# Kernel optimization log

Measured on AMD Instinct MI355X. Metric: run time of the kernel, lower is better.

## Reference

```python
import jax, jax.numpy as jnp
import numpy as np

E = 256      # embedding_dim
H = 16       # head_num
D = 16       # qkv_dim
FF = 512     # ff_hidden_dim
L = 5        # encoder_layer_num
B = 4        # batch
N = 256      # node_cnt
EPS = 1e-5   # InstanceNorm eps


def setup_inputs() -> dict:
    key = jax.random.key(0)
    ks = jax.random.split(key, 16)
    s = 0.05

    def nrm(k, shape):
        return jax.random.normal(k, shape, dtype=jnp.float32) * s

    return {
        "data": jax.random.normal(ks[0], (B, N, N), dtype=jnp.float32),
        "node_rand": jax.random.uniform(ks[1], (B, N, 1), dtype=jnp.float32),
        # Cross_Encoder input projections (Linear(1, E))
        "Wnode": nrm(ks[2], (1, E)), "bnode": jnp.zeros((E,), jnp.float32),
        "Wedge": nrm(ks[3], (1, E)), "bedge": jnp.zeros((E,), jnp.float32),
        # Per layer (L) x per block (2: row/col) weights
        "Wq": nrm(ks[4], (L, 2, E, H * D)),
        "Wk": nrm(ks[5], (L, 2, E, H * D)),
        "Wv": nrm(ks[6], (L, 2, E, H * D)),
        "Wcomb": nrm(ks[7], (L, 2, H * D, E)),
        "bcomb": jnp.zeros((L, 2, E), jnp.float32),
        "n1w": jnp.ones((L, 2, E), jnp.float32),
        "n1b": jnp.zeros((L, 2, E), jnp.float32),
        "W1": nrm(ks[8], (L, 2, E, FF)),
        "b1": jnp.zeros((L, 2, FF), jnp.float32),
        "W2": nrm(ks[9], (L, 2, FF, E)),
        "b2": jnp.zeros((L, 2, E), jnp.float32),
        "n2w": jnp.ones((L, 2, E), jnp.float32),
        "n2b": jnp.zeros((L, 2, E), jnp.float32),
        # MixedScore edge-bias projection per block: E -> H channels
        "Wmix": nrm(ks[10], (L, 2, E, H)),
    }


def _instance_norm(x, w, b):
    # x: [B, N, E]; InstanceNorm1d after transpose -> normalize over node dim N per (B, channel)
    mu = jnp.mean(x, axis=1, keepdims=True)
    var = jnp.var(x, axis=1, keepdims=True)
    return (x - mu) * jax.lax.rsqrt(var + EPS) * w + b


def reference(data, node_rand, Wnode, bnode, Wedge, bedge,
              Wq, Wk, Wv, Wcomb, bcomb, n1w, n1b,
              W1, b1, W2, b2, n2w, n2b, Wmix):
    inv_sqrt_d = jnp.float32(1.0) / jnp.sqrt(jnp.float32(D))

    def block(row, col, edge, i, j):
        # row, col: [B, N, E]; edge: [B, N, N, E]
        q = (row @ Wq[i, j]).reshape(B, N, H, D)
        k = (col @ Wk[i, j]).reshape(B, N, H, D)
        v = (col @ Wv[i, j]).reshape(B, N, H, D)
        score = jnp.einsum('bnhd,bmhd->bhnm', q, k) * inv_sqrt_d
        score = score + jnp.einsum('bnme,eh->bhnm', edge, Wmix[i, j])
        w = jax.nn.softmax(score, axis=-1)
        out = jnp.einsum('bhnm,bmhd->bnhd', w, v).reshape(B, N, H * D)
        mh = out @ Wcomb[i, j] + bcomb[i, j]
        o1 = _instance_norm(row + mh, n1w[i, j], n1b[i, j])
        ff = jax.nn.relu(o1 @ W1[i, j] + b1[i, j]) @ W2[i, j] + b2[i, j]
        return _instance_norm(o1 + ff, n2w[i, j], n2b[i, j])

    # compute_normalized_matrices: per-batch global min-max scaling
    flat = data.reshape(B, -1)
    mn = flat.min(axis=1).reshape(B, 1, 1)
    mx = flat.max(axis=1).reshape(B, 1, 1)
    rng = mx - mn
    rng = jnp.where(rng == 0, jnp.float32(1.0), rng)
    scaled = (data - mn) / rng

    edge = scaled[..., None] @ Wedge + bedge           # [B, N, N, E]
    emb = node_rand @ Wnode + bnode                    # [B, N, E]

    row, col = emb, emb
    for i in range(L):
        row_new = block(row, col, edge, i, 0)
        col = block(col, row, jnp.swapaxes(edge, 1, 2), i, 1)
        row = row_new
    return row, col
```

## Files before the change

### kernel.cpp

```cpp
#include <hip/hip_runtime.h>
#include <hip/hip_bf16.h>

#define E 256
#define H 16
#define DD 16
#define FFH 512
#define LAYERS 5
#define BB 4
#define NN 256
#define MROWS 1024

typedef __attribute__((ext_vector_type(8))) short bfrag;
typedef __attribute__((ext_vector_type(4))) float f32x4;
typedef __attribute__((ext_vector_type(8))) unsigned short us8;
typedef unsigned short u16;

__device__ __forceinline__ void bsplit(float v, u16& h, u16& l) {
    unsigned u = __float_as_uint(v);
    u16 hh = (u16)((u + 0x7fffu + ((u >> 16) & 1u)) >> 16);
    float r = v - __uint_as_float((unsigned)hh << 16);
    unsigned u2 = __float_as_uint(r);
    h = hh;
    l = (u16)((u2 + 0x7fffu + ((u2 >> 16) & 1u)) >> 16);
}

union PrepS {
    float tile[32 * 33];
    struct { u16 th[64 * 40], tl[64 * 40]; } wp;
    struct { float smin[4], smax[4]; } mm;
};

__global__ __launch_bounds__(256) void k_prep(
    const float* __restrict__ data, const float* __restrict__ node_rand,
    const float* __restrict__ Wnode, const float* __restrict__ bnode,
    const float* __restrict__ Wedge, const float* __restrict__ bedge,
    const float* __restrict__ Wmix,
    const float* __restrict__ Wq, const float* __restrict__ Wk, const float* __restrict__ Wv,
    const float* __restrict__ Wc, const float* __restrict__ W1, const float* __restrict__ W2,
    float* __restrict__ pmin, float* __restrict__ pmax, float* __restrict__ c1c0,
    float* __restrict__ rowb, float* __restrict__ colb,
    u16* rowh, u16* rowl, u16* colh, u16* coll,
    float* __restrict__ dataT,
    u16* qh, u16* ql, u16* kh, u16* kl_, u16* vh, u16* vl,
    u16* ch, u16* cl, u16* f1h, u16* f1l, u16* f2h, u16* f2l) {
    __shared__ PrepS ps;
    int bid = blockIdx.x;
    int t = threadIdx.x;
    if (bid < 64) {
        int b = bid >> 4, p = bid & 15;
        const float* src = data + (size_t)b * NN * NN + p * 4096;
        float lmin = 1e30f, lmax = -1e30f;
        #pragma unroll
        for (int i = 0; i < 16; i++) {
            float v = src[t + i * 256];
            lmin = fminf(lmin, v);
            lmax = fmaxf(lmax, v);
        }
        #pragma unroll
        for (int off = 32; off; off >>= 1) {
            lmin = fminf(lmin, __shfl_down(lmin, off));
            lmax = fmaxf(lmax, __shfl_down(lmax, off));
        }
        int wid = t >> 6, lane = t & 63;
        if (lane == 0) { ps.mm.smin[wid] = lmin; ps.mm.smax[wid] = lmax; }
        __syncthreads();
        if (t == 0) {
            pmin[b * 16 + p] = fminf(fminf(ps.mm.smin[0], ps.mm.smin[1]), fminf(ps.mm.smin[2], ps.mm.smin[3]));
            pmax[b * 16 + p] = fmaxf(fmaxf(ps.mm.smax[0], ps.mm.smax[1]), fmaxf(ps.mm.smax[2], ps.mm.smax[3]));
        }
    } else if (bid < 1088) {
        int idx = (bid - 64) * 256 + t;
        int bn = idx >> 8, e = idx & 255;
        float v = node_rand[bn] * Wnode[e] + bnode[e];
        rowb[idx] = v;
        colb[idx] = v;
        u16 h, l;
        bsplit(v, h, l);
        rowh[idx] = h; rowl[idx] = l;
        colh[idx] = h; coll[idx] = l;
    } else if (bid < 1344) {
        int local = bid - 1088;
        int bx = local & 7, by = (local >> 3) & 7, b = local >> 6;
        int r0 = by * 32, c0 = bx * 32;
        int tx = t & 31, ty = t >> 5;
        const float* src = data + (size_t)b * NN * NN;
        float* dst = dataT + (size_t)b * NN * NN;
        #pragma unroll
        for (int i = 0; i < 4; i++)
            ps.tile[(ty + 8 * i) * 33 + tx] = src[(size_t)(r0 + ty + 8 * i) * NN + c0 + tx];
        __syncthreads();
        #pragma unroll
        for (int i = 0; i < 4; i++)
            dst[(size_t)(c0 + ty + 8 * i) * NN + r0 + tx] = ps.tile[tx * 33 + ty + 8 * i];
    } else if (bid < 3904) {
        int id = bid - 1344;
        const float* W; u16 *Dh, *Dl; int K, N, mat, s, nt;
        if (id < 1280) {
            int seg = id / 320, local = id % 320;
            mat = local >> 5; int rem = local & 31; s = rem >> 2; nt = rem & 3;
            K = 256; N = 256;
            W  = seg == 0 ? Wq : seg == 1 ? Wk : seg == 2 ? Wv : Wc;
            Dh = seg == 0 ? qh : seg == 1 ? kh : seg == 2 ? vh : ch;
            Dl = seg == 0 ? ql : seg == 1 ? kl_ : seg == 2 ? vl : cl;
        } else if (id < 1920) {
            int local = id - 1280;
            mat = local >> 6; int rem = local & 63; s = rem >> 3; nt = rem & 7;
            K = 256; N = 512; W = W1; Dh = f1h; Dl = f1l;
        } else {
            int local = id - 1920;
            mat = local >> 6; int rem = local & 63; s = rem >> 2; nt = rem & 3;
            K = 512; N = 256; W = W2; Dh = f2h; Dl = f2l;
        }
        int kk = t >> 3, nl = (t & 7) * 8;
        const float* p = W + (size_t)mat * K * N + (size_t)(s * 32 + kk) * N + nt * 64 + nl;
        float4 f0 = *(const float4*)p;
        float4 f1v = *(const float4*)(p + 4);
        float fv[8] = {f0.x, f0.y, f0.z, f0.w, f1v.x, f1v.y, f1v.z, f1v.w};
        #pragma unroll
        for (int i = 0; i < 8; i++) bsplit(fv[i], ps.wp.th[(nl + i) * 40 + kk], ps.wp.tl[(nl + i) * 40 + kk]);
        __syncthreads();
        int n = t >> 2, ko = (t & 3) * 8;
        size_t dbase = (size_t)mat * K * N + (size_t)s * N * 32 + (size_t)nt * 64 * 32
                     + (size_t)n * 32 + ko;
        *(us8*)(Dh + dbase) = *(const us8*)&ps.wp.th[n * 40 + ko];
        *(us8*)(Dl + dbase) = *(const us8*)&ps.wp.tl[n * 40 + ko];
    } else {
        if (t < LAYERS * 2 * H) {
            int lj = t >> 4, h = t & 15;
            float c1 = 0.f, c0 = 0.f;
            for (int e = 0; e < E; e++) {
                float wm = Wmix[(lj * E + e) * H + h];
                c1 += Wedge[e] * wm;
                c0 += bedge[e] * wm;
            }
            c1c0[t] = c1;
            c1c0[160 + t] = c0;
        }
    }
}

__device__ __forceinline__ void mfma_gemm(const u16* __restrict__ Ah, const u16* __restrict__ Al,
                                          const u16* __restrict__ Bh, const u16* __restrict__ Bl,
                                          const float* __restrict__ bias, const float* __restrict__ R,
                                          float* __restrict__ Cf, u16* __restrict__ Ch,
                                          u16* __restrict__ Cl, int K, int Ncols, int relu) {
    __shared__ u16 AsH[32 * 136], AsL[32 * 136], BsH[64 * 136], BsL[64 * 136];
    int t = threadIdx.x;
    int lane = t & 63, wave = t >> 6;
    int quad = lane >> 4, l16 = lane & 15;
    int wy = wave >> 1, wx = wave & 1;
    int mBase = blockIdx.x * 32, nBase = blockIdx.y * 64;
    f32x4 acc0 = {0.f, 0.f, 0.f, 0.f}, acc1 = acc0;
    int arow = t >> 3, ak = (t & 7) * 16;
    int bcol = lane, bq = wave;
    const int nslab = K >> 7;
    const u16* apH = Ah + (size_t)(mBase + arow) * K + ak;
    const u16* apL = Al + (size_t)(mBase + arow) * K + ak;
    const size_t sstr = (size_t)Ncols * 32;
    size_t bbase = (size_t)bq * sstr + (size_t)(nBase + bcol) * 32;
    const u16* bpH = Bh + bbase;
    const u16* bpL = Bl + bbase;
    us8 rah0 = *(const us8*)apH, rah1 = *(const us8*)(apH + 8);
    us8 ral0 = *(const us8*)apL, ral1 = *(const us8*)(apL + 8);
    us8 rbh0 = *(const us8*)(bpH + 0);
    us8 rbh1 = *(const us8*)(bpH + 8);
    us8 rbh2 = *(const us8*)(bpH + 16);
    us8 rbh3 = *(const us8*)(bpH + 24);
    us8 rbl0 = *(const us8*)(bpL + 0);
    us8 rbl1 = *(const us8*)(bpL + 8);
    us8 rbl2 = *(const us8*)(bpL + 16);
    us8 rbl3 = *(const us8*)(bpL + 24);
    for (int s = 0; s < nslab; s++) {
        __syncthreads();
        *(us8*)&AsH[arow * 136 + ak] = rah0;  *(us8*)&AsH[arow * 136 + ak + 8] = rah1;
        *(us8*)&AsL[arow * 136 + ak] = ral0;  *(us8*)&AsL[arow * 136 + ak + 8] = ral1;
        {
            int bb = bcol * 136 + bq * 32;
            *(us8*)&BsH[bb + 0] = rbh0;  *(us8*)&BsH[bb + 8] = rbh1;
            *(us8*)&BsH[bb + 16] = rbh2; *(us8*)&BsH[bb + 24] = rbh3;
            *(us8*)&BsL[bb + 0] = rbl0;  *(us8*)&BsL[bb + 8] = rbl1;
            *(us8*)&BsL[bb + 16] = rbl2; *(us8*)&BsL[bb + 24] = rbl3;
        }
        __syncthreads();
        if (s + 1 < nslab) {
            rah0 = *(const us8*)(apH + (s + 1) * 128);
            rah1 = *(const us8*)(apH + (s + 1) * 128 + 8);
            ral0 = *(const us8*)(apL + (s + 1) * 128);
            ral1 = *(const us8*)(apL + (s + 1) * 128 + 8);
            const u16* nbH = bpH + (size_t)(4 * (s + 1)) * sstr;
            const u16* nbL = bpL + (size_t)(4 * (s + 1)) * sstr;
            rbh0 = *(const us8*)(nbH + 0);  rbh1 = *(const us8*)(nbH + 8);
            rbh2 = *(const us8*)(nbH + 16); rbh3 = *(const us8*)(nbH + 24);
            rbl0 = *(const us8*)(nbL + 0);  rbl1 = *(const us8*)(nbL + 8);
            rbl2 = *(const us8*)(nbL + 16); rbl3 = *(const us8*)(nbL + 24);
        }
        #pragma unroll
        for (int c = 0; c < 4; c++) {
            bfrag a_h = *(const bfrag*)&AsH[(wy * 16 + l16) * 136 + c * 32 + quad * 8];
            bfrag a_l = *(const bfrag*)&AsL[(wy * 16 + l16) * 136 + c * 32 + quad * 8];
            bfrag b_h0 = *(const bfrag*)&BsH[(wx * 32 + l16) * 136 + c * 32 + quad * 8];
            bfrag b_h1 = *(const bfrag*)&BsH[(wx * 32 + 16 + l16) * 136 + c * 32 + quad * 8];
            bfrag b_l0 = *(const bfrag*)&BsL[(wx * 32 + l16) * 136 + c * 32 + quad * 8];
            bfrag b_l1 = *(const bfrag*)&BsL[(wx * 32 + 16 + l16) * 136 + c * 32 + quad * 8];
            acc0 = __builtin_amdgcn_mfma_f32_16x16x32_bf16(a_h, b_h0, acc0, 0, 0, 0);
            acc1 = __builtin_amdgcn_mfma_f32_16x16x32_bf16(a_h, b_h1, acc1, 0, 0, 0);
            acc0 = __builtin_amdgcn_mfma_f32_16x16x32_bf16(a_h, b_l0, acc0, 0, 0, 0);
            acc1 = __builtin_amdgcn_mfma_f32_16x16x32_bf16(a_h, b_l1, acc1, 0, 0, 0);
            acc0 = __builtin_amdgcn_mfma_f32_16x16x32_bf16(a_l, b_h0, acc0, 0, 0, 0);
            acc1 = __builtin_amdgcn_mfma_f32_16x16x32_bf16(a_l, b_h1, acc1, 0, 0, 0);
        }
    }
    int col0 = nBase + wx * 32 + l16;
    int col1 = col0 + 16;
    float bia0 = bias ? bias[col0] : 0.f;
    float bia1 = bias ? bias[col1] : 0.f;
    #pragma unroll
    for (int r = 0; r < 4; r++) {
        int row0 = mBase + wy * 16 + quad * 4 + r;
        float v0 = acc0[r] + bia0, v1 = acc1[r] + bia1;
        if (R) {
            v0 += R[(size_t)row0 * Ncols + col0];
            v1 += R[(size_t)row0 * Ncols + col1];
        }
        if (relu) {
            v0 = fmaxf(v0, 0.f); v1 = fmaxf(v1, 0.f);
        }
        if (Cf) {
            Cf[(size_t)row0 * Ncols + col0] = v0;
            Cf[(size_t)row0 * Ncols + col1] = v1;
        } else {
            u16 h, l;
            bsplit(v0, h, l); Ch[(size_t)row0 * Ncols + col0] = h; Cl[(size_t)row0 * Ncols + col0] = l;
            bsplit(v1, h, l); Ch[(size_t)row0 * Ncols + col1] = h; Cl[(size_t)row0 * Ncols + col1] = l;
        }
    }
}

__global__ __launch_bounds__(256) void k_qkv(const u16* __restrict__ rowh, const u16* __restrict__ rowl,
                                             const u16* __restrict__ colh, const u16* __restrict__ coll,
                                             const u16* __restrict__ WqTh, const u16* __restrict__ WqTl,
                                             const u16* __restrict__ WkTh, const u16* __restrict__ WkTl,
                                             const u16* __restrict__ WvTh, const u16* __restrict__ WvTl,
                                             int lb2,
                                             u16* qhh0, u16* qhl0, u16* khh0, u16* khl0, u16* vhh0, u16* vhl0,
                                             u16* qhh1, u16* qhl1, u16* khh1, u16* khl1, u16* vhh1, u16* vhl1) {
    int z = blockIdx.z;
    int j = z / 3, w = z % 3;
    const u16* Ah = (w == 0) ? (j ? colh : rowh) : (j ? rowh : colh);
    const u16* Al = (w == 0) ? (j ? coll : rowl) : (j ? rowl : coll);
    const u16* Wh = (w == 0 ? WqTh : (w == 1 ? WkTh : WvTh)) + (size_t)(lb2 + j) * E * E;
    const u16* Wl = (w == 0 ? WqTl : (w == 1 ? WkTl : WvTl)) + (size_t)(lb2 + j) * E * E;
    u16* outs_h[6] = {qhh0, khh0, vhh0, qhh1, khh1, vhh1};
    u16* outs_l[6] = {qhl0, khl0, vhl0, qhl1, khl1, vhl1};
    mfma_gemm(Ah, Al, Wh, Wl, nullptr, nullptr, nullptr, outs_h[z], outs_l[z], E, E, 0);
}

__global__ __launch_bounds__(256) void k_mgemm(const u16* Ah0, const u16* Al0,
                                               const u16* Ah1, const u16* Al1,
                                               const u16* __restrict__ Bh, const u16* __restrict__ Bl,
                                               int lb2, long wstride,
                                               const float* __restrict__ biasl, int bstride,
                                               const float* R0, const float* R1,
                                               float* Cf0, float* Cf1,
                                               u16* Ch0, u16* Cl0, u16* Ch1, u16* Cl1,
                                               int K, int Ncols, int relu) {
    int j = blockIdx.z;
    mfma_gemm(j ? Ah1 : Ah0, j ? Al1 : Al0,
              Bh + (size_t)(lb2 + j) * wstride, Bl + (size_t)(lb2 + j) * wstride,
              biasl ? biasl + (size_t)j * bstride : nullptr,
              R0 ? (j ? R1 : R0) : nullptr,
              Cf0 ? (j ? Cf1 : Cf0) : nullptr,
              Ch0 ? (j ? Ch1 : Ch0) : nullptr,
              Cl0 ? (j ? Cl1 : Cl0) : nullptr,
              K, Ncols, relu);
}

__global__ __launch_bounds__(256) void k_attn(
    const u16* __restrict__ qh0, const u16* __restrict__ ql0,
    const u16* __restrict__ kh0, const u16* __restrict__ kl0,
    const u16* __restrict__ vh0, const u16* __restrict__ vl0,
    const u16* __restrict__ qh1, const u16* __restrict__ ql1,
    const u16* __restrict__ kh1, const u16* __restrict__ kl1,
    const u16* __restrict__ vh1, const u16* __restrict__ vl1,
    const float* __restrict__ data, const float* __restrict__ dataT,
    const float* __restrict__ pmin, const float* __restrict__ pmax,
    const float* __restrict__ c1c0, int lj_base,
    u16* __restrict__ atth0, u16* __restrict__ attl0,
    u16* __restrict__ atth1, u16* __restrict__ attl1) {
    __shared__ u16 Ks[256 * 40];
    __shared__ u16 VTh[16 * 264];
    __shared__ u16 VTl[16 * 264];
    __shared__ u16 Pw[4][2 * 16 * 40];

    int wgid = blockIdx.x;
    int r8 = wgid & 7;
    int qd = wgid >> 3;
    int nq = qd & 3;
    int bhj = r8 * 16 + (qd >> 2);
    int bh = bhj >> 1;
    int j = bhj & 1;
    int b = bh >> 4, h = bh & 15;
    const u16* qh = j ? qh1 : qh0;
    const u16* ql = j ? ql1 : ql0;
    const u16* kh = j ? kh1 : kh0;
    const u16* kl = j ? kl1 : kl0;
    const u16* vh = j ? vh1 : vh0;
    const u16* vl = j ? vl1 : vl0;
    float mn = 1e30f, mx = -1e30f;
    #pragma unroll
    for (int p = 0; p < 16; p++) {
        mn = fminf(mn, pmin[b * 16 + p]);
        mx = fmaxf(mx, pmax[b * 16 + p]);
    }
    float rng = mx - mn;
    if (rng == 0.f) rng = 1.f;
    float inv = 1.f / rng;
    float c1p = inv * c1c0[(lj_base + j) * 16 + h];
    float c0p = c1c0[160 + (lj_base + j) * 16 + h] - mn * c1p;

    int t = threadIdx.x;
    int lane = t & 63, w = t >> 6;
    int l16 = lane & 15, g = lane >> 4;
    int nb = nq * 64 + w * 16;
    int n = nb + l16;

    bfrag qbh, qbl;
    {
        size_t qoff = ((size_t)(b * NN + n) * E) + h * DD + (g & 1) * 8;
        qbh = *(const bfrag*)(qh + qoff);
        if (g < 2) {
            qbl = *(const bfrag*)(ql + qoff);
        } else {
            qbl = (bfrag)(short)0;
        }
    }

    {
        size_t roff = ((size_t)(b * NN + t) * E) + h * DD;
        us8 a = *(const us8*)(kh + roff);
        us8 bv = *(const us8*)(kh + roff + 8);
        us8 c = *(const us8*)(kl + roff);
        us8 d = *(const us8*)(kl + roff + 8);
        *(us8*)&Ks[t * 40 + 0] = a;   *(us8*)&Ks[t * 40 + 8] = bv;
        *(us8*)&Ks[t * 40 + 16] = c;  *(us8*)&Ks[t * 40 + 24] = d;
        us8 vh0v = *(const us8*)(vh + roff);
        us8 vh1v = *(const us8*)(vh + roff + 8);
        us8 vl0v = *(const us8*)(vl + roff);
        us8 vl1v = *(const us8*)(vl + roff + 8);
        #pragma unroll
        for (int d2 = 0; d2 < 8; d2++) {
            VTh[d2 * 264 + t] = vh0v[d2];
            VTh[(d2 + 8) * 264 + t] = vh1v[d2];
            VTl[d2 * 264 + t] = vl0v[d2];
            VTl[(d2 + 8) * 264 + t] = vl1v[d2];
        }
    }
    __syncthreads();

    const float* pedge = (j ? dataT : data) + (size_t)b * NN * NN + (size_t)n * NN;
    u16* myPh = &Pw[w][0];
    u16* myPl = &Pw[w][16 * 40];
    f32x4 oacc = {0.f, 0.f, 0.f, 0.f};
    float sum = 0.f;
    int aoff = g * 8;

    for (int c = 0; c < 8; c++) {
        #pragma unroll
        for (int tt = 0; tt < 2; tt++) {
            int mt = c * 2 + tt;
            int mrow = mt * 16 + l16;
            bfrag a1 = *(const bfrag*)&Ks[mrow * 40 + aoff];
            f32x4 sacc = {0.f, 0.f, 0.f, 0.f};
            sacc = __builtin_amdgcn_mfma_f32_16x16x32_bf16(a1, qbh, sacc, 0, 0, 0);
            sacc = __builtin_amdgcn_mfma_f32_16x16x32_bf16(a1, qbl, sacc, 0, 0, 0);
            float4 ev = *(const float4*)&pedge[mt * 16 + g * 4];
            float evf[4] = {ev.x, ev.y, ev.z, ev.w};
            u16 ph[4], pl[4];
            #pragma unroll
            for (int r = 0; r < 4; r++) {
                float s = sacc[r] * 0.25f + evf[r] * c1p + c0p;
                float e = __expf(s);
                sum += e;
                bsplit(e, ph[r], pl[r]);
            }
            ushort4 phv; phv.x = ph[0]; phv.y = ph[1]; phv.z = ph[2]; phv.w = ph[3];
            ushort4 plv; plv.x = pl[0]; plv.y = pl[1]; plv.z = pl[2]; plv.w = pl[3];
            *(ushort4*)&myPh[l16 * 40 + tt * 16 + g * 4] = phv;
            *(ushort4*)&myPl[l16 * 40 + tt * 16 + g * 4] = plv;
        }
        bfrag pbh = *(const bfrag*)&myPh[l16 * 40 + g * 8];
        bfrag pbl = *(const bfrag*)&myPl[l16 * 40 + g * 8];
        bfrag vah = *(const bfrag*)&VTh[l16 * 264 + c * 32 + g * 8];
        bfrag vaL = *(const bfrag*)&VTl[l16 * 264 + c * 32 + g * 8];
        oacc = __builtin_amdgcn_mfma_f32_16x16x32_bf16(vah, pbh, oacc, 0, 0, 0);
        oacc = __builtin_amdgcn_mfma_f32_16x16x32_bf16(vah, pbl, oacc, 0, 0, 0);
        oacc = __builtin_amdgcn_mfma_f32_16x16x32_bf16(vaL, pbh, oacc, 0, 0, 0);
    }
    sum += __shfl_xor(sum, 16);
    sum += __shfl_xor(sum, 32);
    float invs = 1.f / sum;
    u16 hh[4], ll[4];
    #pragma unroll
    for (int r = 0; r < 4; r++) bsplit(oacc[r] * invs, hh[r], ll[r]);
    size_t obase = ((size_t)(b * NN + n) * E) + h * DD + g * 4;
    u16* oh = (j ? atth1 : atth0) + obase;
    u16* ol = (j ? attl1 : attl0) + obase;
    ushort4 ohv; ohv.x = hh[0]; ohv.y = hh[1]; ohv.z = hh[2]; ohv.w = hh[3];
    ushort4 olv; olv.x = ll[0]; olv.y = ll[1]; olv.z = ll[2]; olv.w = ll[3];
    *(ushort4*)oh = ohv;
    *(ushort4*)ol = olv;
}

__global__ __launch_bounds__(256) void k_inorm(const float* __restrict__ Y0, const float* __restrict__ Y1,
                                               const float* __restrict__ wl, const float* __restrict__ bl,
                                               int pstride,
                                               float* Of0, float* Of1,
                                               u16* Oh0, u16* Ol0, u16* Oh1, u16* Ol1,
                                               float* __restrict__ fout) {
    int b = blockIdx.x, j = blockIdx.y;
    int ec = blockIdx.z * 8;
    const float* Y = (j ? Y1 : Y0) + (size_t)b * NN * E;
    float* O = (j ? Of1 : Of0) + (size_t)b * NN * E;
    u16* Oh = (j ? Oh1 : Oh0) + (size_t)b * NN * E;
    u16* Ol = (j ? Ol1 : Ol0) + (size_t)b * NN * E;
    const float* w = wl + (size_t)j * pstride;
    const float* bb = bl + (size_t)j * pstride;
    int t = threadIdx.x;
    int et = t & 7, n0 = t >> 3;
    int e = ec + et;
    float vals[8];
    float s = 0.f, s2 = 0.f;
    #pragma unroll
    for (int kk = 0; kk < 8; kk++) {
        float v = Y[(size_t)(n0 + 32 * kk) * E + e];
        vals[kk] = v;
        s += v;
        s2 += v * v;
    }
    __shared__ float ps[32 * 9], ps2[32 * 9];
    ps[n0 * 9 + et] = s;
    ps2[n0 * 9 + et] = s2;
    __syncthreads();
    float st = 0.f, st2 = 0.f;
    #pragma unroll
    for (int kk = 0; kk < 32; kk++) { st += ps[kk * 9 + et]; st2 += ps2[kk * 9 + et]; }
    float mu = st * (1.f / NN);
    float var = fmaxf(st2 * (1.f / NN) - mu * mu, 0.f);
    float scale = w[e] * rsqrtf(var + 1e-5f);
    float shift = bb[e] - mu * scale;
    #pragma unroll
    for (int kk = 0; kk < 8; kk++) {
        float vv = vals[kk] * scale + shift;
        size_t idx = (size_t)(n0 + 32 * kk) * E + e;
        O[idx] = vv;
        u16 hh, ll;
        bsplit(vv, hh, ll);
        Oh[idx] = hh;
        Ol[idx] = ll;
        if (fout) fout[(size_t)j * (BB * NN * E) + (size_t)b * NN * E + idx] = vv;
    }
}


extern "C" void kernel_launch(void* const* d_in, const int* in_sizes, int n_in,
                              void* d_out, int out_size, void* d_ws, size_t ws_size,
                              hipStream_t stream) {
    const float* data      = (const float*)d_in[0];
    const float* node_rand = (const float*)d_in[1];
    const float* Wnode     = (const float*)d_in[2];
    const float* bnode     = (const float*)d_in[3];
    const float* Wedge     = (const float*)d_in[4];
    const float* bedge     = (const float*)d_in[5];
    const float* Wq        = (const float*)d_in[6];
    const float* Wk        = (const float*)d_in[7];
    const float* Wv        = (const float*)d_in[8];
    const float* Wcomb     = (const float*)d_in[9];
    const float* bcomb     = (const float*)d_in[10];
    const float* n1w       = (const float*)d_in[11];
    const float* n1b       = (const float*)d_in[12];
    const float* W1        = (const float*)d_in[13];
    const float* b1        = (const float*)d_in[14];
    const float* W2        = (const float*)d_in[15];
    const float* b2        = (const float*)d_in[16];
    const float* n2w       = (const float*)d_in[17];
    const float* n2b       = (const float*)d_in[18];
    const float* Wmix      = (const float*)d_in[19];
    float* out = (float*)d_out;

    float* ws = (float*)d_ws;
    const size_t T = (size_t)MROWS * E;
    const size_t TF = (size_t)MROWS * FFH;
    float* dataT = ws + 0 * T;
    float* row   = ws + 1 * T;
    float* col   = ws + 2 * T;
    float* q0    = ws + 3 * T;
    float* q1    = ws + 4 * T;
    float* o1f0  = ws + 9 * T;
    float* o1f1  = ws + 10 * T;
    float* pmin  = ws + 11 * T;
    float* pmax  = pmin + 64;
    float* c1c0  = pmax + 64;
    u16* us = (u16*)(ws + 11 * T + 512);
    auto nxt = [&](size_t n) { u16* p = us; us += n; return p; };
    u16* rowh = nxt(T);  u16* rowl = nxt(T);
    u16* colh = nxt(T);  u16* coll = nxt(T);
    u16* atth0 = nxt(T); u16* attl0 = nxt(T);
    u16* atth1 = nxt(T); u16* attl1 = nxt(T);
    u16* o1h0 = nxt(T);  u16* o1l0 = nxt(T);
    u16* o1h1 = nxt(T);  u16* o1l1 = nxt(T);
    u16* ffhh0 = nxt(TF); u16* ffhl0 = nxt(TF);
    u16* ffhh1 = nxt(TF); u16* ffhl1 = nxt(TF);
    const size_t EE10 = (size_t)10 * E * E;
    const size_t EF10 = (size_t)10 * E * FFH;
    u16* WqTh = nxt(EE10); u16* WqTl = nxt(EE10);
    u16* WkTh = nxt(EE10); u16* WkTl = nxt(EE10);
    u16* WvTh = nxt(EE10); u16* WvTl = nxt(EE10);
    u16* WcTh = nxt(EE10); u16* WcTl = nxt(EE10);
    u16* W1Th = nxt(EF10); u16* W1Tl = nxt(EF10);
    u16* W2Th = nxt(EF10); u16* W2Tl = nxt(EF10);
    u16* qhh0 = nxt(T); u16* qhl0 = nxt(T);
    u16* khh0 = nxt(T); u16* khl0 = nxt(T);
    u16* vhh0 = nxt(T); u16* vhl0 = nxt(T);
    u16* qhh1 = nxt(T); u16* qhl1 = nxt(T);
    u16* khh1 = nxt(T); u16* khl1 = nxt(T);
    u16* vhh1 = nxt(T); u16* vhl1 = nxt(T);
    float* y0 = q0;   float* y1 = q1;
    float* y20 = q0;  float* y21 = q1;

    k_prep<<<3905, 256, 0, stream>>>(data, node_rand, Wnode, bnode,
                                     Wedge, bedge, Wmix,
                                     Wq, Wk, Wv, Wcomb, W1, W2,
                                     pmin, pmax, c1c0,
                                     row, col, rowh, rowl, colh, coll, dataT,
                                     WqTh, WqTl, WkTh, WkTl, WvTh, WvTl,
                                     WcTh, WcTl, W1Th, W1Tl, W2Th, W2Tl);

    for (int l = 0; l < LAYERS; l++) {
        int lb2 = l * 2;
        k_qkv<<<dim3(32, 4, 6), 256, 0, stream>>>(rowh, rowl, colh, coll,
                                                  WqTh, WqTl, WkTh, WkTl, WvTh, WvTl, lb2,
                                                  qhh0, qhl0, khh0, khl0, vhh0, vhl0,
                                                  qhh1, qhl1, khh1, khl1, vhh1, vhl1);
        k_attn<<<dim3(512), 256, 0, stream>>>(qhh0, qhl0, khh0, khl0, vhh0, vhl0,
                                              qhh1, qhl1, khh1, khl1, vhh1, vhl1,
                                              data, dataT, pmin, pmax, c1c0, lb2,
                                              atth0, attl0, atth1, attl1);
        k_mgemm<<<dim3(32, 4, 2), 256, 0, stream>>>(atth0, attl0, atth1, attl1,
                                                    WcTh, WcTl, lb2, (long)E * E,
                                                    bcomb, E,
                                                    row, col, y0, y1,
                                                    nullptr, nullptr, nullptr, nullptr,
                                                    E, E, 0);
        k_inorm<<<dim3(BB, 2, 32), 256, 0, stream>>>(y0, y1,
                                                     n1w + (size_t)lb2 * E, n1b + (size_t)lb2 * E, E,
                                                     o1f0, o1f1, o1h0, o1l0, o1h1, o1l1, nullptr);
        k_mgemm<<<dim3(32, 8, 2), 256, 0, stream>>>(o1h0, o1l0, o1h1, o1l1,
                                                    W1Th, W1Tl, lb2, (long)E * FFH,
                                                    b1, FFH,
                                                    nullptr, nullptr, nullptr, nullptr,
                                                    ffhh0, ffhl0, ffhh1, ffhl1,
                                                    E, FFH, 1);
        k_mgemm<<<dim3(32, 4, 2), 256, 0, stream>>>(ffhh0, ffhl0, ffhh1, ffhl1,
                                                    W2Th, W2Tl, lb2, (long)FFH * E,
                                                    b2, E,
                                                    o1f0, o1f1, q0 , q1 ,
                                                    nullptr, nullptr, nullptr, nullptr,
                                                    FFH, E, 0);
        k_inorm<<<dim3(BB, 2, 32), 256, 0, stream>>>(y20, y21,
                                                     n2w + (size_t)lb2 * E, n2b + (size_t)lb2 * E, E,
                                                     row, col, rowh, rowl, colh, coll,
                                                     (l == LAYERS - 1) ? out : nullptr);
    }
}
```

Before: 370.6 us.

## Fuse output-projection GEMMs with InstanceNorm into single per-batch kernel

Adds k_gin, which runs the Wcomb and W2 GEMMs with each block owning every node row of one batch and 16 output columns, so the InstanceNorm statistics over the node dimension are reduced inside the block. The fp32 intermediate round trip and the two separate k_inorm launches per layer go away. In exchange the grid shrinks to 128 blocks, and A and B fragments are loaded straight from global memory with no LDS staging, so the GEMM part may run slower than the tiled k_mgemm.

```diff
diff --git a/kernel.cpp b/kernel.cpp
--- a/kernel.cpp
+++ b/kernel.cpp
@@ -275,6 +275,93 @@
               K, Ncols, relu);
 }
 
+__global__ __launch_bounds__(256) void k_gin(
+    const u16* Ah0, const u16* Al0, const u16* Ah1, const u16* Al1,
+    const u16* __restrict__ Bh, const u16* __restrict__ Bl,
+    int lb2, long wstride,
+    const float* __restrict__ biasl, int bstride,
+    const float* R0, const float* R1,
+    const float* __restrict__ wl, const float* __restrict__ bnl,
+    float* Of0, float* Of1,
+    u16* Oh0, u16* Ol0, u16* Oh1, u16* Ol1,
+    float* __restrict__ fout, int K) {
+    int et = blockIdx.x, b = blockIdx.y, j = blockIdx.z;
+    int ec = et * 16;
+    const u16* Ah = (j ? Ah1 : Ah0) + (size_t)b * NN * K;
+    const u16* Al = (j ? Al1 : Al0) + (size_t)b * NN * K;
+    const u16* Bhp = Bh + (size_t)(lb2 + j) * wstride;
+    const u16* Blp = Bl + (size_t)(lb2 + j) * wstride;
+    const float* R = (j ? R1 : R0) + (size_t)b * NN * E;
+    float* O = (j ? Of1 : Of0) + (size_t)b * NN * E;
+    u16* Oh = (j ? Oh1 : Oh0) + (size_t)b * NN * E;
+    u16* Ol = (j ? Ol1 : Ol0) + (size_t)b * NN * E;
+    int t = threadIdx.x, lane = t & 63, w = t >> 6;
+    int l16 = lane & 15, g = lane >> 4;
+    int nslab = K >> 5;
+    int col = ec + l16;
+    int nt = ec >> 6;
+    int colw = (ec & 63) + l16;
+    const size_t sstr = (size_t)E * 32;
+    size_t bb0 = (size_t)nt * (64 * 32) + (size_t)colw * 32 + (size_t)g * 8;
+
+    f32x4 acc[4] = {};
+    for (int s = 0; s < nslab; s++) {
+        bfrag bfh = *(const bfrag*)(Bhp + bb0 + (size_t)s * sstr);
+        bfrag bfl = *(const bfrag*)(Blp + bb0 + (size_t)s * sstr);
+        #pragma unroll
+        for (int rt = 0; rt < 4; rt++) {
+            int arow = w * 64 + rt * 16 + l16;
+            const u16* aph = Ah + (size_t)arow * K + s * 32 + g * 8;
+            const u16* apl = Al + (size_t)arow * K + s * 32 + g * 8;
+            bfrag a_h = *(const bfrag*)aph;
+            bfrag a_l = *(const bfrag*)apl;
+            acc[rt] = __builtin_amdgcn_mfma_f32_16x16x32_bf16(a_h, bfh, acc[rt], 0, 0, 0);
+            acc[rt] = __builtin_amdgcn_mfma_f32_16x16x32_bf16(a_h, bfl, acc[rt], 0, 0, 0);
+            acc[rt] = __builtin_amdgcn_mfma_f32_16x16x32_bf16(a_l, bfh, acc[rt], 0, 0, 0);
+        }
+    }
+    float bias = biasl ? biasl[(size_t)(lb2 + j) * bstride + col] : 0.f;
+    float v[4][4];
+    float s1 = 0.f, s2 = 0.f;
+    #pragma unroll
+    for (int rt = 0; rt < 4; rt++) {
+        #pragma unroll
+        for (int r = 0; r < 4; r++) {
+            int row = w * 64 + rt * 16 + g * 4 + r;
+            float vv = acc[rt][r] + bias + R[(size_t)row * E + col];
+            v[rt][r] = vv;
+            s1 += vv;
+            s2 += vv * vv;
+        }
+    }
+    s1 += __shfl_xor(s1, 16); s2 += __shfl_xor(s2, 16);
+    s1 += __shfl_xor(s1, 32); s2 += __shfl_xor(s2, 32);
+    __shared__ float red1[4][20], red2[4][20];
+    if (lane < 16) { red1[w][l16] = s1; red2[w][l16] = s2; }
+    __syncthreads();
+    float st = red1[0][l16] + red1[1][l16] + red1[2][l16] + red1[3][l16];
+    float st2 = red2[0][l16] + red2[1][l16] + red2[2][l16] + red2[3][l16];
+    float mu = st * (1.f / NN);
+    float var = fmaxf(st2 * (1.f / NN) - mu * mu, 0.f);
+    float scale = wl[(size_t)j * E + col] * rsqrtf(var + 1e-5f);
+    float shift = bnl[(size_t)j * E + col] - mu * scale;
+    #pragma unroll
+    for (int rt = 0; rt < 4; rt++) {
+        #pragma unroll
+        for (int r = 0; r < 4; r++) {
+            int row = w * 64 + rt * 16 + g * 4 + r;
+            float vv = v[rt][r] * scale + shift;
+            size_t idx = (size_t)row * E + col;
+            O[idx] = vv;
+            u16 hh, ll;
+            bsplit(vv, hh, ll);
+            Oh[idx] = hh;
+            Ol[idx] = ll;
+            if (fout) fout[(size_t)j * (BB * NN * E) + (size_t)b * NN * E + idx] = vv;
+        }
+    }
+}
+
 __global__ __launch_bounds__(256) void k_attn(
     const u16* __restrict__ qh0, const u16* __restrict__ ql0,
     const u16* __restrict__ kh0, const u16* __restrict__ kl0,
@@ -409,56 +496,6 @@
     ushort4 olv; olv.x = ll[0]; olv.y = ll[1]; olv.z = ll[2]; olv.w = ll[3];
     *(ushort4*)oh = ohv;
     *(ushort4*)ol = olv;
-}
-
-__global__ __launch_bounds__(256) void k_inorm(const float* __restrict__ Y0, const float* __restrict__ Y1,
-                                               const float* __restrict__ wl, const float* __restrict__ bl,
-                                               int pstride,
-                                               float* Of0, float* Of1,
-                                               u16* Oh0, u16* Ol0, u16* Oh1, u16* Ol1,
-                                               float* __restrict__ fout) {
-    int b = blockIdx.x, j = blockIdx.y;
-    int ec = blockIdx.z * 8;
-    const float* Y = (j ? Y1 : Y0) + (size_t)b * NN * E;
-    float* O = (j ? Of1 : Of0) + (size_t)b * NN * E;
-    u16* Oh = (j ? Oh1 : Oh0) + (size_t)b * NN * E;
-    u16* Ol = (j ? Ol1 : Ol0) + (size_t)b * NN * E;
-    const float* w = wl + (size_t)j * pstride;
-    const float* bb = bl + (size_t)j * pstride;
-    int t = threadIdx.x;
-    int et = t & 7, n0 = t >> 3;
-    int e = ec + et;
-    float vals[8];
-    float s = 0.f, s2 = 0.f;
-    #pragma unroll
-    for (int kk = 0; kk < 8; kk++) {
-        float v = Y[(size_t)(n0 + 32 * kk) * E + e];
-        vals[kk] = v;
-        s += v;
-        s2 += v * v;
-    }
-    __shared__ float ps[32 * 9], ps2[32 * 9];
-    ps[n0 * 9 + et] = s;
-    ps2[n0 * 9 + et] = s2;
-    __syncthreads();
-    float st = 0.f, st2 = 0.f;
-    #pragma unroll
-    for (int kk = 0; kk < 32; kk++) { st += ps[kk * 9 + et]; st2 += ps2[kk * 9 + et]; }
-    float mu = st * (1.f / NN);
-    float var = fmaxf(st2 * (1.f / NN) - mu * mu, 0.f);
-    float scale = w[e] * rsqrtf(var + 1e-5f);
-    float shift = bb[e] - mu * scale;
-    #pragma unroll
-    for (int kk = 0; kk < 8; kk++) {
-        float vv = vals[kk] * scale + shift;
-        size_t idx = (size_t)(n0 + 32 * kk) * E + e;
-        O[idx] = vv;
-        u16 hh, ll;
-        bsplit(vv, hh, ll);
-        Oh[idx] = hh;
-        Ol[idx] = ll;
-        if (fout) fout[(size_t)j * (BB * NN * E) + (size_t)b * NN * E + idx] = vv;
-    }
 }
 
 
@@ -493,8 +530,6 @@
     float* dataT = ws + 0 * T;
     float* row   = ws + 1 * T;
     float* col   = ws + 2 * T;
-    float* q0    = ws + 3 * T;
-    float* q1    = ws + 4 * T;
     float* o1f0  = ws + 9 * T;
     float* o1f1  = ws + 10 * T;
     float* pmin  = ws + 11 * T;
@@ -524,8 +559,6 @@
     u16* qhh1 = nxt(T); u16* qhl1 = nxt(T);
     u16* khh1 = nxt(T); u16* khl1 = nxt(T);
     u16* vhh1 = nxt(T); u16* vhl1 = nxt(T);
-    float* y0 = q0;   float* y1 = q1;
-    float* y20 = q0;  float* y21 = q1;
 
     k_prep<<<3905, 256, 0, stream>>>(data, node_rand, Wnode, bnode,
                                      Wedge, bedge, Wmix,
@@ -545,30 +578,25 @@
                                               qhh1, qhl1, khh1, khl1, vhh1, vhl1,
                                               data, dataT, pmin, pmax, c1c0, lb2,
                                               atth0, attl0, atth1, attl1);
-        k_mgemm<<<dim3(32, 4, 2), 256, 0, stream>>>(atth0, attl0, atth1, attl1,
-                                                    WcTh, WcTl, lb2, (long)E * E,
-                                                    bcomb, E,
-                                                    row, col, y0, y1,
-                                                    nullptr, nullptr, nullptr, nullptr,
-                                                    E, E, 0);
-        k_inorm<<<dim3(BB, 2, 32), 256, 0, stream>>>(y0, y1,
-                                                     n1w + (size_t)lb2 * E, n1b + (size_t)lb2 * E, E,
-                                                     o1f0, o1f1, o1h0, o1l0, o1h1, o1l1, nullptr);
+        k_gin<<<dim3(16, BB, 2), 256, 0, stream>>>(atth0, attl0, atth1, attl1,
+                                                   WcTh, WcTl, lb2, (long)E * E,
+                                                   bcomb, E,
+                                                   row, col,
+                                                   n1w + (size_t)lb2 * E, n1b + (size_t)lb2 * E,
+                                                   o1f0, o1f1, o1h0, o1l0, o1h1, o1l1,
+                                                   nullptr, E);
         k_mgemm<<<dim3(32, 8, 2), 256, 0, stream>>>(o1h0, o1l0, o1h1, o1l1,
                                                     W1Th, W1Tl, lb2, (long)E * FFH,
                                                     b1, FFH,
                                                     nullptr, nullptr, nullptr, nullptr,
                                                     ffhh0, ffhl0, ffhh1, ffhl1,
                                                     E, FFH, 1);
-        k_mgemm<<<dim3(32, 4, 2), 256, 0, stream>>>(ffhh0, ffhl0, ffhh1, ffhl1,
-                                                    W2Th, W2Tl, lb2, (long)FFH * E,
-                                                    b2, E,
-                                                    o1f0, o1f1, q0 , q1 ,
-                                                    nullptr, nullptr, nullptr, nullptr,
-                                                    FFH, E, 0);
-        k_inorm<<<dim3(BB, 2, 32), 256, 0, stream>>>(y20, y21,
-                                                     n2w + (size_t)lb2 * E, n2b + (size_t)lb2 * E, E,
-                                                     row, col, rowh, rowl, colh, coll,
-                                                     (l == LAYERS - 1) ? out : nullptr);
-    }
-}
+        k_gin<<<dim3(16, BB, 2), 256, 0, stream>>>(ffhh0, ffhl0, ffhh1, ffhl1,
+                                                   W2Th, W2Tl, lb2, (long)FFH * E,
+                                                   b2, E,
+                                                   o1f0, o1f1,
+                                                   n2w + (size_t)lb2 * E, n2b + (size_t)lb2 * E,
+                                                   row, col, rowh, rowl, colh, coll,
+                                                   (l == LAYERS - 1) ? out : nullptr, FFH);
+    }
+}
```

New measurement: 412.3 us. 11.3% more time.
